# Optimization experiments

Hardware: AMD Instinct MI355X
Metric: run time of the kernel (lower is better)

Reference implementation:

```python
import jax, jax.numpy as jnp
import numpy as np

B, S, D, H = 8, 1024, 1024, 16
DK = D // H


def setup_inputs() -> dict:
    key = jax.random.key(0)
    ks = jax.random.split(key, 12)
    sc = 1.0 / np.sqrt(D)
    return {
        "query": jax.random.normal(ks[0], (B, S, D), jnp.float32),
        "key": jax.random.normal(ks[1], (B, S, D), jnp.float32),
        "value": jax.random.normal(ks[2], (B, S, D), jnp.float32),
        "Wq": jax.random.normal(ks[3], (D, D), jnp.float32) * sc,
        "bq": jnp.zeros((D,), jnp.float32),
        "Wk": jax.random.normal(ks[4], (D, D), jnp.float32) * sc,
        "bk": jnp.zeros((D,), jnp.float32),
        "Wv": jax.random.normal(ks[5], (D, D), jnp.float32) * sc,
        "bv": jnp.zeros((D,), jnp.float32),
        "Wa": jax.random.normal(ks[6], (D, D), jnp.float32) * sc,
        "ba": jnp.zeros((D,), jnp.float32),
        "qvec": jax.random.normal(ks[7], (D,), jnp.float32),
    }


def reference(query, key, value, Wq, bq, Wk, bk, Wv, bv, Wa, ba, qvec):
    # project and split heads: [B,S,D] -> [B,H,S,DK]
    def split(x, W, b):
        y = x @ W.T + b
        return y.reshape(B, S, H, DK).transpose(0, 2, 1, 3)

    q = split(query, Wq, bq)
    k = split(key, Wk, bk)
    v = split(value, Wv, bv)

    scores = jnp.einsum('bhqd,bhkd->bhqk', q, k) / jnp.sqrt(jnp.float32(DK))
    p = jax.nn.softmax(scores, axis=-1)          # dropout p=0 -> identity
    x = jnp.einsum('bhqk,bhkd->bhqd', p, v)
    x = x.transpose(0, 2, 1, 3).reshape(B, S, D)  # [B,S,D]

    # attention2 pooling head
    a = jnp.tanh(x @ Wa.T + ba) @ qvec           # [B,S]
    alpha = jax.nn.softmax(a, axis=-1)
    return jnp.einsum('bs,bsd->bd', alpha, x)    # [B,D]
```

## Files before the change

kernel.cpp:

```cpp
#include <hip/hip_runtime.h>

typedef __bf16 bf16;
typedef __attribute__((ext_vector_type(8))) __bf16 bf16x8;
typedef __attribute__((ext_vector_type(4))) __bf16 bf16x4;
typedef __attribute__((ext_vector_type(4))) float f32x4;

#define GLDS16(g, l) __builtin_amdgcn_global_load_lds( \
    (const __attribute__((address_space(1))) void*)(g), \
    (__attribute__((address_space(3))) void*)(l), 16, 0, 0)

#define MFMA16(a, b, c) __builtin_amdgcn_mfma_f32_16x16x32_bf16(a, b, c, 0, 0, 0)

#define TR16(dst, addr, off) \
  asm volatile("ds_read_b64_tr_b16 %0, %1 offset:" #off : "=v"(dst) : "v"(addr))

struct CvtArgs { const float* in[4]; bf16* out[4]; };

__global__ __launch_bounds__(256) void f2b_multi(CvtArgs a, int n8) {
  int i = blockIdx.x * 256 + threadIdx.x;
  if (i >= n8) return;
  const float* in = a.in[blockIdx.y];
  bf16* out = a.out[blockIdx.y];
  const f32x4* p = (const f32x4*)in + (size_t)i * 2;
  f32x4 x = p[0], y = p[1];
  bf16x8 o;
  o[0] = (bf16)x[0]; o[1] = (bf16)x[1]; o[2] = (bf16)x[2]; o[3] = (bf16)x[3];
  o[4] = (bf16)y[0]; o[5] = (bf16)y[1]; o[6] = (bf16)y[2]; o[7] = (bf16)y[3];
  ((bf16x8*)out)[i] = o;
}

template <int EPI>
__device__ __forceinline__ void gemm_body8(
    const bf16* __restrict__ A, const bf16* __restrict__ Bw,
    const float* __restrict__ bias, const float* __restrict__ qv,
    bf16* __restrict__ C, float* __restrict__ aout,
    const int row0, const int col0, const int N, const int K) {
  __shared__ __attribute__((aligned(16))) bf16 L[2][4][8192];
  const int tid = threadIdx.x;
  const int wid = tid >> 6, lane = tid & 63;
  const int g = lane >> 4, lc = lane & 15;
  const int wr = wid >> 2, wc = wid & 3;

  const bf16* gA = A + (size_t)(row0 + (tid & 255)) * K + (tid >> 8) * 8;
  const bf16* gB = Bw + (size_t)(col0 + (tid & 255)) * K + (tid >> 8) * 8;
  const int d0 = (tid - lane) * 8;

#define STG_A(T, kh) do { \
    const bf16* gp_ = gA + (T) * 64 + (kh) * 32; \
    bf16* lp_ = &L[(T) & 1][(kh)][d0]; \
    GLDS16(gp_, lp_); GLDS16(gp_ + 16, lp_ + 4096); } while (0)
#define STG_B(T, kh) do { \
    const bf16* gp_ = gB + (T) * 64 + (kh) * 32; \
    bf16* lp_ = &L[(T) & 1][2 + (kh)][d0]; \
    GLDS16(gp_, lp_); GLDS16(gp_ + 16, lp_ + 4096); } while (0)
#define RD_A(c, kh) do { \
    _Pragma("unroll") for (int m_ = 0; m_ < 8; ++m_) \
      af[m_] = *(const bf16x8*)&L[c][kh][(g * 256 + wr * 128 + m_ * 16 + lc) * 8]; \
  } while (0)
#define RD_B(c, kh, nh) do { \
    bf[0] = *(const bf16x8*)&L[c][2 + (kh)][(g * 256 + wc * 64 + (nh) * 32 + lc) * 8]; \
    bf[1] = *(const bf16x8*)&L[c][2 + (kh)][(g * 256 + wc * 64 + (nh) * 32 + 16 + lc) * 8]; \
  } while (0)
#define BARS \
    __builtin_amdgcn_s_barrier(); \
    asm volatile("s_waitcnt lgkmcnt(0)" ::: "memory"); \
    __builtin_amdgcn_sched_barrier(0);
#define MM(nh) do { \
    __builtin_amdgcn_s_setprio(1); \
    _Pragma("unroll") for (int m_ = 0; m_ < 8; ++m_) { \
      acc[m_][(nh) * 2 + 0] = MFMA16(af[m_], bf[0], acc[m_][(nh) * 2 + 0]); \
      acc[m_][(nh) * 2 + 1] = MFMA16(af[m_], bf[1], acc[m_][(nh) * 2 + 1]); \
    } \
    __builtin_amdgcn_s_setprio(0); } while (0)
#define ENDP __builtin_amdgcn_s_barrier();

  const f32x4 z4 = {0.f, 0.f, 0.f, 0.f};
  f32x4 acc[8][4];
#pragma unroll
  for (int m = 0; m < 8; ++m)
#pragma unroll
    for (int n = 0; n < 4; ++n) acc[m][n] = z4;

  bf16x8 af[8], bf[2];
  const int NT = K >> 6;
  const int NI = NT >> 1;

  STG_A(0, 0); STG_B(0, 0); STG_A(0, 1); STG_B(0, 1);
  STG_A(1, 0); STG_B(1, 0); STG_A(1, 1);
  asm volatile("s_waitcnt vmcnt(6)" ::: "memory");
  __builtin_amdgcn_s_barrier();

  for (int i = 0; i < NI; ++i) {
    const int t1 = 2 * i + 1, t2 = 2 * i + 2, t3 = 2 * i + 3;
    const bool p2 = t2 < NT, p3 = t3 < NT;
    RD_A(0, 0); RD_B(0, 0, 0);
    STG_B(t1, 1);
    BARS; MM(0); ENDP;
    RD_B(0, 0, 1);
    if (p2) STG_A(t2, 0);
    BARS; MM(1); ENDP;
    RD_A(0, 1); RD_B(0, 1, 0);
    if (p2) STG_B(t2, 0);
    BARS; MM(0); ENDP;
    RD_B(0, 1, 1);
    if (p2) STG_A(t2, 1);
    BARS; MM(1);
    if (p2) { asm volatile("s_waitcnt vmcnt(6)" ::: "memory"); }
    else    { asm volatile("s_waitcnt vmcnt(0)" ::: "memory"); }
    ENDP;
    RD_A(1, 0); RD_B(1, 0, 0);
    if (p2) STG_B(t2, 1);
    BARS; MM(0); ENDP;
    RD_B(1, 0, 1);
    if (p3) STG_A(t3, 0);
    BARS; MM(1); ENDP;
    RD_A(1, 1); RD_B(1, 1, 0);
    if (p3) STG_B(t3, 0);
    BARS; MM(0); ENDP;
    RD_B(1, 1, 1);
    if (p3) STG_A(t3, 1);
    BARS; MM(1);
    asm volatile("s_waitcnt vmcnt(6)" ::: "memory");
    ENDP;
  }

#undef STG_A
#undef STG_B
#undef RD_A
#undef RD_B
#undef BARS
#undef MM
#undef ENDP

  if constexpr (EPI == 0) {
#pragma unroll
    for (int n = 0; n < 4; ++n) {
      const int col = col0 + wc * 64 + n * 16 + lc;
      const float bb = bias[col];
#pragma unroll
      for (int m = 0; m < 8; ++m)
#pragma unroll
        for (int r = 0; r < 4; ++r) {
          const int row = row0 + wr * 128 + m * 16 + g * 4 + r;
          C[(size_t)row * N + col] = (bf16)(acc[m][n][r] + bb);
        }
    }
  } else {
    float part[8][4];
#pragma unroll
    for (int m = 0; m < 8; ++m)
#pragma unroll
      for (int r = 0; r < 4; ++r) part[m][r] = 0.f;
#pragma unroll
    for (int n = 0; n < 4; ++n) {
      const int col = col0 + wc * 64 + n * 16 + lc;
      const float bb = bias[col];
      const float qq = qv[col];
#pragma unroll
      for (int m = 0; m < 8; ++m)
#pragma unroll
        for (int r = 0; r < 4; ++r)
          part[m][r] += tanhf(acc[m][n][r] + bb) * qq;
    }
#pragma unroll
    for (int m = 0; m < 8; ++m)
#pragma unroll
      for (int r = 0; r < 4; ++r) {
        float v = part[m][r];
        v += __shfl_xor(v, 1); v += __shfl_xor(v, 2);
        v += __shfl_xor(v, 4); v += __shfl_xor(v, 8);
        if (lc == 0) {
          const int row = row0 + wr * 128 + m * 16 + g * 4 + r;
          atomicAdd(&aout[row], v);
        }
      }
  }
}

__device__ __forceinline__ void swz128(int phys, int& row0, int& col0) {
  const int lg = (phys & 7) * 16 + (phys >> 3);
  row0 = (lg >> 2) * 256;
  col0 = (lg & 3) * 256;
}

struct GemmSet { const bf16* A; const bf16* Bw; const float* bias; bf16* C; };
struct Gemm3Args { GemmSet s[3]; };

__global__ __launch_bounds__(512, 2) void gemm3_kernel(Gemm3Args a) {
  const GemmSet s = a.s[blockIdx.y];
  int row0, col0;
  swz128(blockIdx.x, row0, col0);
  gemm_body8<0>(s.A, s.Bw, s.bias, nullptr, s.C, nullptr, row0, col0, 1024, 1024);
}

__global__ __launch_bounds__(512, 2) void gemm_a_kernel(
    const bf16* __restrict__ A, const bf16* __restrict__ Bw,
    const float* __restrict__ bias, const float* __restrict__ qv,
    float* __restrict__ aout) {
  int row0, col0;
  swz128(blockIdx.x, row0, col0);
  gemm_body8<1>(A, Bw, bias, qv, nullptr, aout, row0, col0, 1024, 1024);
}

__global__ __launch_bounds__(256) void attn_kernel(
    const bf16* __restrict__ qp, const bf16* __restrict__ kp,
    const bf16* __restrict__ vp, bf16* __restrict__ xb, float* __restrict__ xf) {
  constexpr int S = 1024, D = 1024;
  __shared__ __attribute__((aligned(16))) bf16 Ks[8192];
  __shared__ __attribute__((aligned(16))) bf16 Vs[8192];
  __shared__ __attribute__((aligned(16))) bf16 Ps[4096];
  const int tid = threadIdx.x, wid = tid >> 6, lane = tid & 63;
  const int g = lane >> 4, lc = lane & 15;
  const int b = blockIdx.x >> 4, h = blockIdx.x & 15;
  const int q0 = blockIdx.y * 64;
  const size_t base = (size_t)b * S * D + (size_t)h * 64;

  bf16x8 qf[2];
  {
    const bf16* qrow = qp + base + (size_t)(q0 + wid * 16 + lc) * D;
    qf[0] = *(const bf16x8*)(qrow + g * 8);
    qf[1] = *(const bf16x8*)(qrow + 32 + g * 8);
#pragma unroll
    for (int j = 0; j < 8; ++j) {
      qf[0][j] = (bf16)((float)qf[0][j] * 0.125f);
      qf[1][j] = (bf16)((float)qf[1][j] * 0.125f);
    }
  }
  float m_s = -1e30f, l_s = 0.f;
  const f32x4 z4 = {0.f, 0.f, 0.f, 0.f};
  f32x4 ax[4];
#pragma unroll
  for (int m = 0; m < 4; ++m) ax[m] = z4;

  const int c0 = tid, c1 = tid + 256;
  const bf16* gK0 = kp + base + (size_t)(c0 & 63) * D + (c0 >> 6) * 8;
  const bf16* gK1 = kp + base + (size_t)(c1 & 63) * D + (c1 >> 6) * 8;
  bf16* lK0 = Ks + (size_t)(c0 - lane) * 8;
  bf16* lK1 = Ks + (size_t)(c1 - lane) * 8;
  const bf16* gV0 = vp + base + (size_t)((c0 >> 5) * 4 + ((c0 >> 1) & 3)) * D +
                    ((c0 >> 3) & 3) * 16 + (c0 & 1) * 8;
  const bf16* gV1 = vp + base + (size_t)((c1 >> 5) * 4 + ((c1 >> 1) & 3)) * D +
                    ((c1 >> 3) & 3) * 16 + (c1 & 1) * 8;
  bf16* lV0 = Vs + (size_t)(c0 - lane) * 8;
  bf16* lV1 = Vs + (size_t)(c1 - lane) * 8;

  bf16* pw = Ps + wid * 1024;
  const int pswz_a = lc & 3, pswz_b = (lc >> 2) & 3;
  const unsigned vaddr0 =
      (unsigned)(uintptr_t)(const __attribute__((address_space(3))) bf16*)(Vs + 512 * g + 4 * lc);

  GLDS16(gK0, lK0);
  GLDS16(gK1, lK1);
  GLDS16(gV0, lV0);
  GLDS16(gV1, lV1);

  for (int t = 0; t < 16; ++t) {
    __syncthreads();
    const int cur = t & 1;
    if (t < 15) {
      const size_t off = (size_t)(t + 1) * 64 * D;
      const int nb = cur ^ 1;
      GLDS16(gK0 + off, lK0 + nb * 4096);
      GLDS16(gK1 + off, lK1 + nb * 4096);
      GLDS16(gV0 + off, lV0 + nb * 4096);
      GLDS16(gV1 + off, lV1 + nb * 4096);
    }
    const bf16* Kb = Ks + cur * 4096;
    const unsigned va = vaddr0 + cur * 8192u;

    f32x4 sc[4];
    __builtin_amdgcn_s_setprio(1);
#pragma unroll
    for (int m = 0; m < 4; ++m) {
      f32x4 z = z4;
      bf16x8 kf0 = *(const bf16x8*)(Kb + (size_t)g * 512 + (m * 16 + lc) * 8);
      bf16x8 kf1 = *(const bf16x8*)(Kb + (size_t)(4 + g) * 512 + (m * 16 + lc) * 8);
      z = MFMA16(kf0, qf[0], z);
      z = MFMA16(kf1, qf[1], z);
      sc[m] = z;
    }
    __builtin_amdgcn_s_setprio(0);

    float mx = -1e30f;
#pragma unroll
    for (int m = 0; m < 4; ++m)
      mx = fmaxf(mx, fmaxf(fmaxf(sc[m][0], sc[m][1]), fmaxf(sc[m][2], sc[m][3])));
    mx = fmaxf(mx, __shfl_xor(mx, 16));
    mx = fmaxf(mx, __shfl_xor(mx, 32));
    if (!__all(mx - m_s <= 8.f)) {
      const float mn = fmaxf(m_s, mx);
      const float cr = __expf(m_s - mn);
      l_s *= cr;
#pragma unroll
      for (int m = 0; m < 4; ++m) ax[m] *= cr;
      m_s = mn;
    }
    float sm = 0.f;
#pragma unroll
    for (int m = 0; m < 4; ++m)
#pragma unroll
      for (int r = 0; r < 4; ++r) {
        float p = __expf(sc[m][r] - m_s);
        sc[m][r] = p;
        sm += p;
      }
    sm += __shfl_xor(sm, 16);
    sm += __shfl_xor(sm, 32);
    l_s += sm;

#pragma unroll
    for (int m = 0; m < 4; ++m) {
      bf16x4 pk;
      pk[0] = (bf16)sc[m][0]; pk[1] = (bf16)sc[m][1];
      pk[2] = (bf16)sc[m][2]; pk[3] = (bf16)sc[m][3];
      *(bf16x4*)(pw + lc * 64 + 16 * (m ^ pswz_a) + 4 * (g ^ pswz_b)) = pk;
    }

    bf16x4 pr[2][2];
#pragma unroll
    for (int kk = 0; kk < 2; ++kk)
#pragma unroll
      for (int jh = 0; jh < 2; ++jh) {
        const int msrc = 2 * kk + (g >> 1);
        const int gsrc = (2 * g + jh) & 3;
        pr[kk][jh] = *(const bf16x4*)(pw + lc * 64 + 16 * (msrc ^ pswz_a) + 4 * (gsrc ^ pswz_b));
      }
    bf16x8 pf0 = __builtin_shufflevector(pr[0][0], pr[0][1], 0, 1, 2, 3, 4, 5, 6, 7);
    bf16x8 pf1 = __builtin_shufflevector(pr[1][0], pr[1][1], 0, 1, 2, 3, 4, 5, 6, 7);

    bf16x4 vt[4][2][2];
    TR16(vt[0][0][0], va, 0);    TR16(vt[1][0][0], va, 128);
    TR16(vt[2][0][0], va, 256);  TR16(vt[3][0][0], va, 384);
    TR16(vt[0][0][1], va, 512);  TR16(vt[1][0][1], va, 640);
    TR16(vt[2][0][1], va, 768);  TR16(vt[3][0][1], va, 896);
    TR16(vt[0][1][0], va, 4096); TR16(vt[1][1][0], va, 4224);
    TR16(vt[2][1][0], va, 4352); TR16(vt[3][1][0], va, 4480);
    TR16(vt[0][1][1], va, 4608); TR16(vt[1][1][1], va, 4736);
    TR16(vt[2][1][1], va, 4864); TR16(vt[3][1][1], va, 4992);
    asm volatile("s_waitcnt lgkmcnt(0)" ::: "memory");
    __builtin_amdgcn_sched_barrier(0);

    __builtin_amdgcn_s_setprio(1);
#pragma unroll
    for (int md = 0; md < 4; ++md) {
      bf16x8 a0 = __builtin_shufflevector(vt[md][0][0], vt[md][0][1], 0, 1, 2, 3, 4, 5, 6, 7);
      bf16x8 a1 = __builtin_shufflevector(vt[md][1][0], vt[md][1][1], 0, 1, 2, 3, 4, 5, 6, 7);
      ax[md] = MFMA16(a0, pf0, ax[md]);
      ax[md] = MFMA16(a1, pf1, ax[md]);
    }
    __builtin_amdgcn_s_setprio(0);
  }

  const float inv = 1.0f / l_s;
  const int qrow = q0 + wid * 16 + lc;
  float* xfr = xf + base + (size_t)qrow * D;
  bf16* xbr = xb + base + (size_t)qrow * D;
#pragma unroll
  for (int m = 0; m < 4; ++m) {
    f32x4 vv = ax[m] * inv;
    *(f32x4*)(xfr + 16 * m + 4 * g) = vv;
    bf16x4 bb;
    bb[0] = (bf16)vv[0]; bb[1] = (bf16)vv[1];
    bb[2] = (bf16)vv[2]; bb[3] = (bf16)vv[3];
    *(bf16x4*)(xbr + 16 * m + 4 * g) = bb;
  }
}

__global__ __launch_bounds__(256) void softmax_rows(const float* __restrict__ av,
                                                    float* __restrict__ alpha) {
  const int b = blockIdx.x, t = threadIdx.x;
  __shared__ float red[8];
  f32x4 v = *(const f32x4*)(av + b * 1024 + t * 4);
  float m = fmaxf(fmaxf(v[0], v[1]), fmaxf(v[2], v[3]));
#pragma unroll
  for (int o = 1; o < 64; o <<= 1) m = fmaxf(m, __shfl_xor(m, o));
  if ((t & 63) == 0) red[t >> 6] = m;
  __syncthreads();
  m = fmaxf(fmaxf(red[0], red[1]), fmaxf(red[2], red[3]));
  f32x4 e;
  float s = 0.f;
#pragma unroll
  for (int j = 0; j < 4; ++j) { e[j] = __expf(v[j] - m); s += e[j]; }
#pragma unroll
  for (int o = 1; o < 64; o <<= 1) s += __shfl_xor(s, o);
  if ((t & 63) == 0) red[4 + (t >> 6)] = s;
  __syncthreads();
  const float inv = 1.0f / (red[4] + red[5] + red[6] + red[7]);
  *(f32x4*)(alpha + b * 1024 + t * 4) = e * inv;
}

__global__ __launch_bounds__(256) void pool_kernel(const float* __restrict__ xf,
                                                   const float* __restrict__ alpha,
                                                   float* __restrict__ out) {
  const int b = blockIdx.y, sc = blockIdx.x, t = threadIdx.x;
  f32x4 acc = {0.f, 0.f, 0.f, 0.f};
  const float* xrow = xf + (size_t)b * 1024 * 1024;
  for (int s = sc * 64; s < sc * 64 + 64; ++s) {
    const float al = alpha[b * 1024 + s];
    f32x4 xv = *(const f32x4*)(xrow + (size_t)s * 1024 + t * 4);
    acc += xv * al;
  }
  atomicAdd(&out[b * 1024 + t * 4 + 0], acc[0]);
  atomicAdd(&out[b * 1024 + t * 4 + 1], acc[1]);
  atomicAdd(&out[b * 1024 + t * 4 + 2], acc[2]);
  atomicAdd(&out[b * 1024 + t * 4 + 3], acc[3]);
}

extern "C" void kernel_launch(void* const* d_in, const int* in_sizes, int n_in,
                              void* d_out, int out_size, void* d_ws, size_t ws_size,
                              hipStream_t stream) {
  const float* Q   = (const float*)d_in[0];
  const float* K   = (const float*)d_in[1];
  const float* V   = (const float*)d_in[2];
  const float* Wq  = (const float*)d_in[3];
  const float* bq  = (const float*)d_in[4];
  const float* Wk  = (const float*)d_in[5];
  const float* bk  = (const float*)d_in[6];
  const float* Wv  = (const float*)d_in[7];
  const float* bv  = (const float*)d_in[8];
  const float* Wa  = (const float*)d_in[9];
  const float* ba  = (const float*)d_in[10];
  const float* qvec = (const float*)d_in[11];
  float* out = (float*)d_out;
  char* ws = (char*)d_ws;
  const size_t MB = 1ull << 20;

  bf16* Wqb = (bf16*)(ws + 0 * MB);
  bf16* Wkb = (bf16*)(ws + 2 * MB);
  bf16* Wvb = (bf16*)(ws + 4 * MB);
  bf16* Wab = (bf16*)(ws + 6 * MB);
  bf16* qb  = (bf16*)(ws + 8 * MB);
  bf16* kb  = (bf16*)(ws + 24 * MB);
  bf16* vb  = (bf16*)(ws + 40 * MB);
  bf16* qp  = (bf16*)(ws + 56 * MB);
  bf16* kp  = (bf16*)(ws + 72 * MB);
  bf16* vp  = (bf16*)(ws + 88 * MB);
  float* av    = (float*)(ws + 104 * MB);
  float* alpha = (float*)(ws + 104 * MB + 65536);
  bf16* xb  = qb;
  float* xf = (float*)(ws + 24 * MB);

  hipMemsetAsync(av, 0, 8192 * sizeof(float), stream);
  hipMemsetAsync(out, 0, 8192 * sizeof(float), stream);

  CvtArgs cq = {{Q, K, V, nullptr}, {qb, kb, vb, nullptr}};
  f2b_multi<<<dim3(4096, 3), 256, 0, stream>>>(cq, 1048576);
  CvtArgs cw = {{Wq, Wk, Wv, Wa}, {Wqb, Wkb, Wvb, Wab}};
  f2b_multi<<<dim3(512, 4), 256, 0, stream>>>(cw, 131072);

  Gemm3Args g3 = {{{qb, Wqb, bq, qp}, {kb, Wkb, bk, kp}, {vb, Wvb, bv, vp}}};
  gemm3_kernel<<<dim3(128, 3), 512, 0, stream>>>(g3);

  attn_kernel<<<dim3(128, 16), 256, 0, stream>>>(qp, kp, vp, xb, xf);

  gemm_a_kernel<<<128, 512, 0, stream>>>(xb, Wab, ba, qvec, av);

  softmax_rows<<<8, 256, 0, stream>>>(av, alpha);
  pool_kernel<<<dim3(16, 8), 256, 0, stream>>>(xf, alpha, out);
}
```

Measured before the change: 266.7 us.

## Fuse softmax and pooling, replace atomics with partial buffers, merge conversions

Merges the activation and weight fp32-to-bf16 conversions into one launch and drops both memsets. The pooling-logit GEMM now writes per-column-tile partial sums instead of using atomics. A single kernel then reduces those partials, computes the softmax and does the weighted pooling without atomics. This removes launches and atomic traffic, but the pooling now runs on only 8 blocks, each streaming a 4MB slice serially, which cuts parallelism. It also adds a sched_barrier after GEMM barriers.

Result: slower. 296.8 us (+11.3%).

```diff
diff --git a/kernel.cpp b/kernel.cpp
--- a/kernel.cpp
+++ b/kernel.cpp
@@ -14,26 +14,37 @@
 #define TR16(dst, addr, off) \
   asm volatile("ds_read_b64_tr_b16 %0, %1 offset:" #off : "=v"(dst) : "v"(addr))
 
-struct CvtArgs { const float* in[4]; bf16* out[4]; };
-
-__global__ __launch_bounds__(256) void f2b_multi(CvtArgs a, int n8) {
-  int i = blockIdx.x * 256 + threadIdx.x;
-  if (i >= n8) return;
-  const float* in = a.in[blockIdx.y];
-  bf16* out = a.out[blockIdx.y];
-  const f32x4* p = (const f32x4*)in + (size_t)i * 2;
+struct CvtAll { const float* in[7]; bf16* out[7]; };
+
+__global__ __launch_bounds__(256) void f2b_all(CvtAll a) {
+  const int i = blockIdx.x * 256 + threadIdx.x;
+  const float* in;
+  bf16* out;
+  int off;
+  if (blockIdx.y < 3) {
+    in = a.in[blockIdx.y];
+    out = a.out[blockIdx.y];
+    off = i;
+  } else {
+    if (i >= 524288) return;
+    const int widx = 3 + (i >> 17);
+    in = a.in[widx];
+    out = a.out[widx];
+    off = i & 131071;
+  }
+  const f32x4* p = (const f32x4*)in + (size_t)off * 2;
   f32x4 x = p[0], y = p[1];
   bf16x8 o;
   o[0] = (bf16)x[0]; o[1] = (bf16)x[1]; o[2] = (bf16)x[2]; o[3] = (bf16)x[3];
   o[4] = (bf16)y[0]; o[5] = (bf16)y[1]; o[6] = (bf16)y[2]; o[7] = (bf16)y[3];
-  ((bf16x8*)out)[i] = o;
+  ((bf16x8*)out)[off] = o;
 }
 
 template <int EPI>
 __device__ __forceinline__ void gemm_body8(
     const bf16* __restrict__ A, const bf16* __restrict__ Bw,
     const float* __restrict__ bias, const float* __restrict__ qv,
-    bf16* __restrict__ C, float* __restrict__ aout,
+    bf16* __restrict__ C, float* __restrict__ part,
     const int row0, const int col0, const int N, const int K) {
   __shared__ __attribute__((aligned(16))) bf16 L[2][4][8192];
   const int tid = threadIdx.x;
@@ -72,7 +83,10 @@
       acc[m_][(nh) * 2 + 1] = MFMA16(af[m_], bf[1], acc[m_][(nh) * 2 + 1]); \
     } \
     __builtin_amdgcn_s_setprio(0); } while (0)
-#define ENDP __builtin_amdgcn_s_barrier();
+#define ENDP do { \
+    __builtin_amdgcn_s_barrier(); \
+    asm volatile("" ::: "memory"); \
+    __builtin_amdgcn_sched_barrier(0); } while (0)
 
   const f32x4 z4 = {0.f, 0.f, 0.f, 0.f};
   f32x4 acc[8][4];
@@ -88,7 +102,7 @@
   STG_A(0, 0); STG_B(0, 0); STG_A(0, 1); STG_B(0, 1);
   STG_A(1, 0); STG_B(1, 0); STG_A(1, 1);
   asm volatile("s_waitcnt vmcnt(6)" ::: "memory");
-  __builtin_amdgcn_s_barrier();
+  ENDP;
 
   for (int i = 0; i < NI; ++i) {
     const int t1 = 2 * i + 1, t2 = 2 * i + 2, t3 = 2 * i + 3;
@@ -146,11 +160,11 @@
         }
     }
   } else {
-    float part[8][4];
+    float ps[8][4];
 #pragma unroll
     for (int m = 0; m < 8; ++m)
 #pragma unroll
-      for (int r = 0; r < 4; ++r) part[m][r] = 0.f;
+      for (int r = 0; r < 4; ++r) ps[m][r] = 0.f;
 #pragma unroll
     for (int n = 0; n < 4; ++n) {
       const int col = col0 + wc * 64 + n * 16 + lc;
@@ -160,18 +174,19 @@
       for (int m = 0; m < 8; ++m)
 #pragma unroll
         for (int r = 0; r < 4; ++r)
-          part[m][r] += tanhf(acc[m][n][r] + bb) * qq;
-    }
+          ps[m][r] += tanhf(acc[m][n][r] + bb) * qq;
+    }
+    float* pdst = part + (size_t)((col0 >> 8) * 4 + wc) * 8192;
 #pragma unroll
     for (int m = 0; m < 8; ++m)
 #pragma unroll
       for (int r = 0; r < 4; ++r) {
-        float v = part[m][r];
+        float v = ps[m][r];
         v += __shfl_xor(v, 1); v += __shfl_xor(v, 2);
         v += __shfl_xor(v, 4); v += __shfl_xor(v, 8);
         if (lc == 0) {
           const int row = row0 + wr * 128 + m * 16 + g * 4 + r;
-          atomicAdd(&aout[row], v);
+          pdst[row] = v;
         }
       }
   }
@@ -196,10 +211,10 @@
 __global__ __launch_bounds__(512, 2) void gemm_a_kernel(
     const bf16* __restrict__ A, const bf16* __restrict__ Bw,
     const float* __restrict__ bias, const float* __restrict__ qv,
-    float* __restrict__ aout) {
+    float* __restrict__ part) {
   int row0, col0;
   swz128(blockIdx.x, row0, col0);
-  gemm_body8<1>(A, Bw, bias, qv, nullptr, aout, row0, col0, 1024, 1024);
+  gemm_body8<1>(A, Bw, bias, qv, nullptr, part, row0, col0, 1024, 1024);
 }
 
 __global__ __launch_bounds__(256) void attn_kernel(
@@ -366,12 +381,20 @@
   }
 }
 
-__global__ __launch_bounds__(256) void softmax_rows(const float* __restrict__ av,
-                                                    float* __restrict__ alpha) {
+__global__ __launch_bounds__(256) void alphapool_kernel(
+    const float* __restrict__ part, const float* __restrict__ xf,
+    float* __restrict__ out) {
+  __shared__ float alpha[1024];
+  __shared__ float red[8];
   const int b = blockIdx.x, t = threadIdx.x;
-  __shared__ float red[8];
-  f32x4 v = *(const f32x4*)(av + b * 1024 + t * 4);
-  float m = fmaxf(fmaxf(v[0], v[1]), fmaxf(v[2], v[3]));
+
+  f32x4 a4 = {0.f, 0.f, 0.f, 0.f};
+#pragma unroll
+  for (int p = 0; p < 16; ++p) {
+    const float* pp = part + (size_t)p * 8192 + b * 1024 + t * 4;
+    a4[0] += pp[0]; a4[1] += pp[1]; a4[2] += pp[2]; a4[3] += pp[3];
+  }
+  float m = fmaxf(fmaxf(a4[0], a4[1]), fmaxf(a4[2], a4[3]));
 #pragma unroll
   for (int o = 1; o < 64; o <<= 1) m = fmaxf(m, __shfl_xor(m, o));
   if ((t & 63) == 0) red[t >> 6] = m;
@@ -380,30 +403,22 @@
   f32x4 e;
   float s = 0.f;
 #pragma unroll
-  for (int j = 0; j < 4; ++j) { e[j] = __expf(v[j] - m); s += e[j]; }
+  for (int j = 0; j < 4; ++j) { e[j] = __expf(a4[j] - m); s += e[j]; }
 #pragma unroll
   for (int o = 1; o < 64; o <<= 1) s += __shfl_xor(s, o);
   if ((t & 63) == 0) red[4 + (t >> 6)] = s;
   __syncthreads();
   const float inv = 1.0f / (red[4] + red[5] + red[6] + red[7]);
-  *(f32x4*)(alpha + b * 1024 + t * 4) = e * inv;
-}
-
-__global__ __launch_bounds__(256) void pool_kernel(const float* __restrict__ xf,
-                                                   const float* __restrict__ alpha,
-                                                   float* __restrict__ out) {
-  const int b = blockIdx.y, sc = blockIdx.x, t = threadIdx.x;
-  f32x4 acc = {0.f, 0.f, 0.f, 0.f};
-  const float* xrow = xf + (size_t)b * 1024 * 1024;
-  for (int s = sc * 64; s < sc * 64 + 64; ++s) {
-    const float al = alpha[b * 1024 + s];
-    f32x4 xv = *(const f32x4*)(xrow + (size_t)s * 1024 + t * 4);
-    acc += xv * al;
-  }
-  atomicAdd(&out[b * 1024 + t * 4 + 0], acc[0]);
-  atomicAdd(&out[b * 1024 + t * 4 + 1], acc[1]);
-  atomicAdd(&out[b * 1024 + t * 4 + 2], acc[2]);
-  atomicAdd(&out[b * 1024 + t * 4 + 3], acc[3]);
+  *(f32x4*)(alpha + t * 4) = e * inv;
+  __syncthreads();
+
+  f32x4 acc0 = {0.f, 0.f, 0.f, 0.f}, acc1 = {0.f, 0.f, 0.f, 0.f};
+  const float* xrow = xf + (size_t)b * 1024 * 1024 + t * 4;
+  for (int s2 = 0; s2 < 1024; s2 += 2) {
+    acc0 += alpha[s2] * *(const f32x4*)(xrow + (size_t)s2 * 1024);
+    acc1 += alpha[s2 + 1] * *(const f32x4*)(xrow + (size_t)(s2 + 1) * 1024);
+  }
+  *(f32x4*)(out + b * 1024 + t * 4) = acc0 + acc1;
 }
 
 extern "C" void kernel_launch(void* const* d_in, const int* in_sizes, int n_in,
@@ -435,26 +450,19 @@
   bf16* qp  = (bf16*)(ws + 56 * MB);
   bf16* kp  = (bf16*)(ws + 72 * MB);
   bf16* vp  = (bf16*)(ws + 88 * MB);
-  float* av    = (float*)(ws + 104 * MB);
-  float* alpha = (float*)(ws + 104 * MB + 65536);
+  float* part = (float*)(ws + 104 * MB);
   bf16* xb  = qb;
   float* xf = (float*)(ws + 24 * MB);
 
-  hipMemsetAsync(av, 0, 8192 * sizeof(float), stream);
-  hipMemsetAsync(out, 0, 8192 * sizeof(float), stream);
-
-  CvtArgs cq = {{Q, K, V, nullptr}, {qb, kb, vb, nullptr}};
-  f2b_multi<<<dim3(4096, 3), 256, 0, stream>>>(cq, 1048576);
-  CvtArgs cw = {{Wq, Wk, Wv, Wa}, {Wqb, Wkb, Wvb, Wab}};
-  f2b_multi<<<dim3(512, 4), 256, 0, stream>>>(cw, 131072);
+  CvtAll cv = {{Q, K, V, Wq, Wk, Wv, Wa}, {qb, kb, vb, Wqb, Wkb, Wvb, Wab}};
+  f2b_all<<<dim3(4096, 4), 256, 0, stream>>>(cv);
 
   Gemm3Args g3 = {{{qb, Wqb, bq, qp}, {kb, Wkb, bk, kp}, {vb, Wvb, bv, vp}}};
   gemm3_kernel<<<dim3(128, 3), 512, 0, stream>>>(g3);
 
   attn_kernel<<<dim3(128, 16), 256, 0, stream>>>(qp, kp, vp, xb, xf);
 
-  gemm_a_kernel<<<128, 512, 0, stream>>>(xb, Wab, ba, qvec, av);
-
-  softmax_rows<<<8, 256, 0, stream>>>(av, alpha);
-  pool_kernel<<<dim3(16, 8), 256, 0, stream>>>(xf, alpha, out);
-}
+  gemm_a_kernel<<<128, 512, 0, stream>>>(xb, Wab, ba, qvec, part);
+
+  alphapool_kernel<<<8, 256, 0, stream>>>(part, xf, out);
+}
```
